# Kernel optimization log

Hardware: AMD Instinct MI355X
Metric: run time of the kernel (lower is better)

Reference implementation:

```python
import jax, jax.numpy as jnp
import numpy as np
import math

B, TQ, TK, C, H, DFF = 4, 1024, 1024, 1024, 16, 4096
DK = C // H
EPS = 1e-12


def _mha(x_q, x_kv, wq, bq, wk, bk, wv, bv, wo, bo, mask):
    Bq, Tq, Cq = x_q.shape
    Tk = x_kv.shape[1]
    q = (x_q @ wq + bq).reshape(Bq, Tq, H, DK).transpose(0, 2, 1, 3)  # [B,H,Tq,dk]
    k = (x_kv @ wk + bk).reshape(Bq, Tk, H, DK).transpose(0, 2, 1, 3)
    v = (x_kv @ wv + bv).reshape(Bq, Tk, H, DK).transpose(0, 2, 1, 3)
    scores = jnp.einsum('bhqd,bhkd->bhqk', q, k) * (1.0 / math.sqrt(DK))
    if mask is not None:
        scores = jnp.where(mask, scores, jnp.asarray(-1e9, scores.dtype))
    attn = jax.nn.softmax(scores, axis=-1)
    o = jnp.einsum('bhqk,bhkd->bhqd', attn, v).transpose(0, 2, 1, 3).reshape(Bq, Tq, Cq)
    return o @ wo + bo


def _ln(x, g, b):
    mu = jnp.mean(x, axis=-1, keepdims=True)
    var = jnp.mean(jnp.square(x - mu), axis=-1, keepdims=True)
    return (x - mu) * jax.lax.rsqrt(var + EPS) * g + b


def setup_inputs() -> dict:
    key = jax.random.key(0)
    ks = iter(jax.random.split(key, 32))
    s = 0.02
    inp = {}
    inp['src'] = jax.random.normal(next(ks), (B, TK, C), jnp.float32)
    inp['dst'] = jax.random.normal(next(ks), (B, TQ, C), jnp.float32)
    inp['src_mask'] = jnp.ones((B, 1, 1, TK), dtype=bool)  # key-padding mask (all valid)
    inp['dst_mask'] = jnp.tril(jnp.ones((TQ, TQ), dtype=bool))[None, None]  # causal
    for p in ['sa', 'ca']:
        for n in ['wq', 'wk', 'wv', 'wo']:
            inp[f'{p}_{n}'] = jax.random.normal(next(ks), (C, C), jnp.float32) * s
        for n in ['bq', 'bk', 'bv', 'bo']:
            inp[f'{p}_{n}'] = jnp.zeros((C,), jnp.float32)
    inp['ffn_w1'] = jax.random.normal(next(ks), (C, DFF), jnp.float32) * s
    inp['ffn_b1'] = jnp.zeros((DFF,), jnp.float32)
    inp['ffn_w2'] = jax.random.normal(next(ks), (DFF, C), jnp.float32) * s
    inp['ffn_b2'] = jnp.zeros((C,), jnp.float32)
    for i in ['1', '2', '3']:
        inp[f'ln{i}_g'] = jnp.ones((C,), jnp.float32)
        inp[f'ln{i}_b'] = jnp.zeros((C,), jnp.float32)
    return inp


def reference(src, dst, src_mask, dst_mask,
              sa_wq, sa_wk, sa_wv, sa_wo, sa_bq, sa_bk, sa_bv, sa_bo,
              ca_wq, ca_wk, ca_wv, ca_wo, ca_bq, ca_bk, ca_bv, ca_bo,
              ffn_w1, ffn_b1, ffn_w2, ffn_b2,
              ln1_g, ln1_b, ln2_g, ln2_b, ln3_g, ln3_b):
    # post-LN decoder layer, eval mode (dropout is identity)
    sa = _mha(dst, dst, sa_wq, sa_bq, sa_wk, sa_bk, sa_wv, sa_bv, sa_wo, sa_bo, dst_mask)
    y = _ln(dst + sa, ln1_g, ln1_b)
    ca = _mha(y, src, ca_wq, ca_bq, ca_wk, ca_bk, ca_wv, ca_bv, ca_wo, ca_bo, src_mask)
    y = _ln(y + ca, ln2_g, ln2_b)
    ff = jax.nn.gelu(y @ ffn_w1 + ffn_b1, approximate=False) @ ffn_w2 + ffn_b2
    return _ln(y + ff, ln3_g, ln3_b)
```

## Files before the change

kernel.cpp:

```cpp
#include <hip/hip_runtime.h>
#include <math.h>

typedef __attribute__((ext_vector_type(4))) float f32x4;
typedef __attribute__((ext_vector_type(8))) __bf16 bf16x8;
typedef __attribute__((ext_vector_type(8))) short short8;

#define DEV __device__ __forceinline__

DEV short f2bfs(float f) {
    unsigned u = __builtin_bit_cast(unsigned, f);
    unsigned r = (u + 0x7FFFu + ((u >> 16) & 1u)) >> 16;
    return (short)r;
}

DEV f32x4 mfma16(bf16x8 a, bf16x8 b, f32x4 c) {
    return __builtin_amdgcn_mfma_f32_16x16x32_bf16(a, b, c, 0, 0, 0);
}

DEV void gload_lds16(const void* g, void* l) {
    __builtin_amdgcn_global_load_lds((const __attribute__((address_space(1))) void*)g,
                                     (__attribute__((address_space(3))) void*)l, 16, 0, 0);
}

__global__ __launch_bounds__(256) void wtrans(const float* __restrict__ Win,
                                              short* __restrict__ Wout,
                                              int Kd, int Nd) {
    __shared__ float Tt[32][33];
    const int tx = threadIdx.x & 31, ty = threadIdx.x >> 5;
    const int k0 = blockIdx.y * 32, n0 = blockIdx.x * 32;
#pragma unroll
    for (int rr = 0; rr < 4; ++rr) {
        int k = ty * 4 + rr;
        Tt[k][tx] = Win[(size_t)(k0 + k) * Nd + n0 + tx];
    }
    __syncthreads();
#pragma unroll
    for (int rr = 0; rr < 4; ++rr) {
        int n = ty * 4 + rr;
        Wout[(size_t)(n0 + n) * Kd + k0 + tx] = f2bfs(Tt[tx][n]);
    }
}

struct WPtrs { const float* p[8]; };

__global__ __launch_bounds__(256) void wtrans8(WPtrs wp, short* __restrict__ out) {
    const float* __restrict__ Win = wp.p[blockIdx.z];
    short* __restrict__ Wout = out + (size_t)blockIdx.z * (1024 * 1024);
    __shared__ float Tt[32][33];
    const int tx = threadIdx.x & 31, ty = threadIdx.x >> 5;
    const int k0 = blockIdx.y * 32, n0 = blockIdx.x * 32;
#pragma unroll
    for (int rr = 0; rr < 4; ++rr) {
        int k = ty * 4 + rr;
        Tt[k][tx] = Win[(size_t)(k0 + k) * 1024 + n0 + tx];
    }
    __syncthreads();
#pragma unroll
    for (int rr = 0; rr < 4; ++rr) {
        int n = ty * 4 + rr;
        Wout[(size_t)(n0 + n) * 1024 + k0 + tx] = f2bfs(Tt[tx][n]);
    }
}

__global__ __launch_bounds__(256) void conv_bf16(const float* __restrict__ X,
                                                 short* __restrict__ Y, int n4) {
    int i = blockIdx.x * 256 + threadIdx.x;
    if (i < n4) {
        float4 v = ((const float4*)X)[i];
        short4 o;
        o.x = f2bfs(v.x); o.y = f2bfs(v.y); o.z = f2bfs(v.z); o.w = f2bfs(v.w);
        ((short4*)Y)[i] = o;
    }
}

template <int BM, int BN, int BK, int EPI, bool SWZ>
__global__ __launch_bounds__(256, (BM == 64 && BN == 64) ? 4 : 1)
void gemm_bt(const short* __restrict__ A,
             const short* __restrict__ BT,
             const float* __restrict__ b0,
             const float* __restrict__ b1,
             const float* __restrict__ b2,
             void* __restrict__ o0,
             void* __restrict__ o1,
             void* __restrict__ o2,
             int M, int N, int K, int Ks) {
    constexpr int IM = BM / 32, JN = BN / 32;
    constexpr int KH = BK / 32;
    constexpr int AL = (BM * 64) / 4096;
    constexpr int BL = (BN * 64) / 4096;
    __shared__ __align__(16) short As[2][BM * BK];
    __shared__ __align__(16) short Bs[2][BN * BK];
    const int tid = threadIdx.x, lane = tid & 63, w = tid >> 6;

    int bx, by, bz;
    if (SWZ) {
        int gx = gridDim.x, gy = gridDim.y;
        int G = gx * gy * gridDim.z;
        int fid = blockIdx.x + gx * (blockIdx.y + gy * blockIdx.z);
        int nf = (fid & 7) * (G >> 3) + (fid >> 3);
        bx = nf % gx;
        int t = nf / gx;
        by = t % gy;
        bz = t / gy;
    } else {
        bx = blockIdx.x; by = blockIdx.y; bz = blockIdx.z;
    }

    const int m0 = by * BM, n0 = bx * BN;
    const int kz = bz * K;
    const int wm = (w & 1) * (BM / 2), wn = (w >> 1) * (BN / 2);
    const int rl = lane & 15, rg = lane >> 4;
    f32x4 acc[IM][JN] = {};
    const char* Ab = (const char*)A;
    const char* Bb = (const char*)BT;
    const int nk = K / BK;

    auto stage = [&](int kt, int buf) {
#pragma unroll
        for (int h = 0; h < KH; ++h) {
#pragma unroll
            for (int r = 0; r < AL; ++r) {
                int lo = (tid + r * 256) * 16;
                int row = lo >> 6, cp = (lo >> 4) & 3, c = (cp - (row >> 1)) & 3;
                gload_lds16(Ab + ((size_t)(m0 + row) * Ks + kz + kt * BK + h * 32 + c * 8) * 2,
                            (char*)As[buf] + h * (BM * 64) + lo);
            }
#pragma unroll
            for (int r = 0; r < BL; ++r) {
                int lo = (tid + r * 256) * 16;
                int row = lo >> 6, cp = (lo >> 4) & 3, c = (cp - (row >> 1)) & 3;
                gload_lds16(Bb + ((size_t)(n0 + row) * Ks + kz + kt * BK + h * 32 + c * 8) * 2,
                            (char*)Bs[buf] + h * (BN * 64) + lo);
            }
        }
    };

    stage(0, 0);
    for (int kt = 0; kt < nk; ++kt) {
        const int buf = kt & 1;
        __syncthreads();
        if (kt + 1 < nk) stage(kt + 1, buf ^ 1);
        bf16x8 af[KH][IM], bfr[KH][JN];
#pragma unroll
        for (int h = 0; h < KH; ++h) {
#pragma unroll
            for (int i = 0; i < IM; i++) {
                int row = wm + i * 16 + rl;
                af[h][i] = *(const bf16x8*)(As[buf] + h * (BM * 32) + row * 32 +
                                            ((rg + (row >> 1)) & 3) * 8);
            }
#pragma unroll
            for (int j = 0; j < JN; j++) {
                int row = wn + j * 16 + rl;
                bfr[h][j] = *(const bf16x8*)(Bs[buf] + h * (BN * 32) + row * 32 +
                                             ((rg + (row >> 1)) & 3) * 8);
            }
        }
#pragma unroll
        for (int h = 0; h < KH; ++h)
#pragma unroll
            for (int i = 0; i < IM; i++)
#pragma unroll
                for (int j = 0; j < JN; j++)
                    acc[i][j] = mfma16(af[h][i], bfr[h][j], acc[i][j]);
    }

    float* o0z = (float*)o0 + (size_t)bz * M * N;
#pragma unroll
    for (int i = 0; i < IM; i++) {
        int gm0 = m0 + wm + i * 16 + rg * 4;
#pragma unroll
        for (int j = 0; j < JN; j++) {
            int gn = n0 + wn + j * 16 + rl;
            if (EPI == 0) {
                float bv = bz == 0 ? b0[gn] : 0.0f;
#pragma unroll
                for (int r = 0; r < 4; r++)
                    o0z[(size_t)(gm0 + r) * N + gn] = acc[i][j][r] + bv;
            } else if (EPI == 2) {
                float bv = b0[gn];
#pragma unroll
                for (int r = 0; r < 4; r++) {
                    float x = acc[i][j][r] + bv;
                    float z = 1.59576912f * x + 0.07135481f * x * x * x;
                    float g = x / (1.0f + __expf(-z));
                    ((short*)o0)[(size_t)(gm0 + r) * N + gn] = f2bfs(g);
                }
            } else {
                int seg = gn >> 10, n1 = gn & 1023, h = n1 >> 6, d = n1 & 63;
                int b = gm0 >> 10, t0 = gm0 & 1023;
                bool isV = (EPI == 1) ? (seg == 2) : (seg == 1);
                const float* bp = (EPI == 1) ? (seg == 0 ? b0 : (seg == 1 ? b1 : b2))
                                             : (seg == 0 ? b0 : b1);
                float bv = bp[n1];
                float qs = (EPI == 1 && seg == 0) ? 0.125f : 1.0f;
                if (!isV) {
                    short* hp = (short*)((EPI == 1) ? (seg == 0 ? o0 : o1) : o0);
                    size_t base = ((size_t)(b * 16 + h) * 1024 + t0) * 64 + d;
#pragma unroll
                    for (int r = 0; r < 4; r++)
                        hp[base + (size_t)r * 64] = f2bfs((acc[i][j][r] + bv) * qs);
                } else {
                    short* vp = (short*)((EPI == 1) ? o2 : o1);
                    short4 pk;
                    pk.x = f2bfs(acc[i][j][0] + bv);
                    pk.y = f2bfs(acc[i][j][1] + bv);
                    pk.z = f2bfs(acc[i][j][2] + bv);
                    pk.w = f2bfs(acc[i][j][3] + bv);
                    *(short4*)(vp + ((size_t)(b * 16 + h) * 64 + d) * 1024 + t0) = pk;
                }
            }
        }
    }
}

template <bool CAUSAL>
__global__ __launch_bounds__(256, 3) void attn4(const short* __restrict__ Qh,
                                                const short* __restrict__ Kh,
                                                const short* __restrict__ VTh,
                                                short* __restrict__ Out, int TKn) {
    __shared__ __align__(16) short Ks[2][64 * 64];
    __shared__ __align__(16) short Vts[2][64 * 64];
    __shared__ __align__(16) short Ps[4][16 * 72 + 8];
    const int tid = threadIdx.x, lane = tid & 63, w = tid >> 6;
    const int rl = lane & 15, rg = lane >> 4;
    const int bh = blockIdx.y, b = bh >> 4, h = bh & 15;
    const int q0 = blockIdx.x * 64;
    const short* Qp = Qh + (size_t)bh * 1024 * 64;
    const char* Kp = (const char*)(Kh + (size_t)bh * (size_t)TKn * 64);
    const char* Vp = (const char*)(VTh + (size_t)bh * (size_t)TKn * 64);

    const int qrow = q0 + w * 16 + rl;
    const bf16x8 qf0 = *(const bf16x8*)(Qp + (size_t)qrow * 64 + rg * 8);
    const bf16x8 qf1 = *(const bf16x8*)(Qp + (size_t)qrow * 64 + 32 + rg * 8);

    bf16x8 onesf;
#pragma unroll
    for (int i = 0; i < 8; ++i) onesf[i] = (__bf16)1.0f;

    f32x4 o[4] = {};
    f32x4 lacc = {};

    short* Pw = &Ps[w][0];
    const int nkt = CAUSAL ? blockIdx.x + 1 : (TKn >> 6);

    auto stage = [&](int kt, int buf) {
#pragma unroll
        for (int r = 0; r < 2; ++r) {
            int lo = (w * 2 + r) * 1024 + lane * 16;
            int row = lo >> 7, cp = (lo >> 4) & 7, c = (cp - row) & 7;
            gload_lds16(Kp + ((size_t)(kt * 64 + row) * 64 + c * 8) * 2,
                        (char*)Ks[buf] + lo);
            gload_lds16(Vp + ((size_t)row * TKn + kt * 64 + c * 8) * 2,
                        (char*)Vts[buf] + lo);
        }
    };

    stage(0, 0);
    for (int kt = 0; kt < nkt; ++kt) {
        const int buf = kt & 1;
        __syncthreads();
        if (kt + 1 < nkt) stage(kt + 1, buf ^ 1);

        const short* KsB = Ks[buf];
        f32x4 s[4];
#pragma unroll
        for (int ch = 0; ch < 4; ++ch) {
            int row = ch * 16 + rl;
            bf16x8 k0 = *(const bf16x8*)(KsB + row * 64 + ((rg + row) & 7) * 8);
            bf16x8 k1 = *(const bf16x8*)(KsB + row * 64 + ((rg + 4 + row) & 7) * 8);
            f32x4 z = {};
            z = mfma16(k0, qf0, z);
            z = mfma16(k1, qf1, z);
            s[ch] = z;
        }
        const bool domask = CAUSAL && (kt == nkt - 1);
#pragma unroll
        for (int ch = 0; ch < 4; ++ch) {
            float p[4];
#pragma unroll
            for (int r = 0; r < 4; ++r) {
                float e = __expf(s[ch][r]);
                if (domask) {
                    int key = kt * 64 + ch * 16 + rg * 4 + r;
                    if (key > qrow) e = 0.0f;
                }
                p[r] = e;
            }
            unsigned d0 = (__builtin_bit_cast(unsigned, p[1]) & 0xFFFF0000u) |
                          (__builtin_bit_cast(unsigned, p[0]) >> 16);
            unsigned d1 = (__builtin_bit_cast(unsigned, p[3]) & 0xFFFF0000u) |
                          (__builtin_bit_cast(unsigned, p[2]) >> 16);
            uint2 dv; dv.x = d0; dv.y = d1;
            *(uint2*)(Pw + rl * 72 + ch * 16 + rg * 4) = dv;
        }
        bf16x8 pa0 = *(const bf16x8*)(Pw + rl * 72 + rg * 8);
        bf16x8 pa1 = *(const bf16x8*)(Pw + rl * 72 + 32 + rg * 8);
        lacc = mfma16(pa0, onesf, lacc);
        lacc = mfma16(pa1, onesf, lacc);
        const short* VsB = Vts[buf];
#pragma unroll
        for (int j = 0; j < 4; ++j) {
            int row = j * 16 + rl;
            bf16x8 v0 = *(const bf16x8*)(VsB + row * 64 + ((rg + row) & 7) * 8);
            bf16x8 v1 = *(const bf16x8*)(VsB + row * 64 + ((rg + 4 + row) & 7) * 8);
            o[j] = mfma16(pa0, v0, o[j]);
            o[j] = mfma16(pa1, v1, o[j]);
        }
    }

    float inv[4];
#pragma unroll
    for (int r = 0; r < 4; r++) inv[r] = 1.0f / lacc[r];
#pragma unroll
    for (int j = 0; j < 4; j++) {
#pragma unroll
        for (int r = 0; r < 4; r++) {
            int row = q0 + w * 16 + rg * 4 + r;
            int col = h * 64 + j * 16 + rl;
            Out[((size_t)b * 1024 + row) * 1024 + col] = f2bfs(o[j][r] * inv[r]);
        }
    }
}

__global__ __launch_bounds__(256) void ln_fused(const float* __restrict__ X,
                                                const float* __restrict__ R,
                                                const float* __restrict__ R2,
                                                const float* __restrict__ gam,
                                                const float* __restrict__ bet,
                                                float* __restrict__ Yf,
                                                short* __restrict__ Yb) {
    const int row = blockIdx.x, tid = threadIdx.x;
    const int lane = tid & 63, w = tid >> 6;
    float4 xv = ((const float4*)(X + (size_t)row * 1024))[tid];
    float4 rv = ((const float4*)(R + (size_t)row * 1024))[tid];
    float v0 = xv.x + rv.x, v1 = xv.y + rv.y, v2 = xv.z + rv.z, v3 = xv.w + rv.w;
    if (R2) {
        float4 r2 = ((const float4*)(R2 + (size_t)row * 1024))[tid];
        v0 += r2.x; v1 += r2.y; v2 += r2.z; v3 += r2.w;
    }
    float s = v0 + v1 + v2 + v3;
    float ss = v0 * v0 + v1 * v1 + v2 * v2 + v3 * v3;
#pragma unroll
    for (int off = 1; off < 64; off <<= 1) {
        s += __shfl_xor(s, off);
        ss += __shfl_xor(ss, off);
    }
    __shared__ float sred[4], ssred[4];
    if (lane == 0) { sred[w] = s; ssred[w] = ss; }
    __syncthreads();
    s = sred[0] + sred[1] + sred[2] + sred[3];
    ss = ssred[0] + ssred[1] + ssred[2] + ssred[3];
    float mu = s * (1.0f / 1024.0f);
    float var = ss * (1.0f / 1024.0f) - mu * mu;
    float rsq = rsqrtf(var + 1e-12f);
    float4 gv = ((const float4*)gam)[tid];
    float4 bv = ((const float4*)bet)[tid];
    float y0 = (v0 - mu) * rsq * gv.x + bv.x;
    float y1 = (v1 - mu) * rsq * gv.y + bv.y;
    float y2 = (v2 - mu) * rsq * gv.z + bv.z;
    float y3 = (v3 - mu) * rsq * gv.w + bv.w;
    float4 yo = {y0, y1, y2, y3};
    ((float4*)(Yf + (size_t)row * 1024))[tid] = yo;
    if (Yb) {
        short4 ob;
        ob.x = f2bfs(y0); ob.y = f2bfs(y1); ob.z = f2bfs(y2); ob.w = f2bfs(y3);
        ((short4*)(Yb + (size_t)row * 1024))[tid] = ob;
    }
}

extern "C" void kernel_launch(void* const* d_in, const int* in_sizes, int n_in,
                              void* d_out, int out_size, void* d_ws, size_t ws_size,
                              hipStream_t stream) {
    const float* src = (const float*)d_in[0];
    const float* dst = (const float*)d_in[1];
    const float* sa_wq = (const float*)d_in[4];
    const float* sa_wk = (const float*)d_in[5];
    const float* sa_wv = (const float*)d_in[6];
    const float* sa_wo = (const float*)d_in[7];
    const float* sa_bq = (const float*)d_in[8];
    const float* sa_bk = (const float*)d_in[9];
    const float* sa_bv = (const float*)d_in[10];
    const float* sa_bo = (const float*)d_in[11];
    const float* ca_wq = (const float*)d_in[12];
    const float* ca_wk = (const float*)d_in[13];
    const float* ca_wv = (const float*)d_in[14];
    const float* ca_wo = (const float*)d_in[15];
    const float* ca_bq = (const float*)d_in[16];
    const float* ca_bk = (const float*)d_in[17];
    const float* ca_bv = (const float*)d_in[18];
    const float* ca_bo = (const float*)d_in[19];
    const float* ffn_w1 = (const float*)d_in[20];
    const float* ffn_b1 = (const float*)d_in[21];
    const float* ffn_w2 = (const float*)d_in[22];
    const float* ffn_b2 = (const float*)d_in[23];
    const float* ln1g = (const float*)d_in[24];
    const float* ln1b = (const float*)d_in[25];
    const float* ln2g = (const float*)d_in[26];
    const float* ln2b = (const float*)d_in[27];
    const float* ln3g = (const float*)d_in[28];
    const float* ln3b = (const float*)d_in[29];

    char* ws = (char*)d_ws;
    size_t off = 0;
    auto alloc = [&](size_t n) { size_t o = off; off = (off + n + 255) & ~(size_t)255; return o; };

    const size_t szW = (size_t)1024 * 1024 * 2;
    short* wT = (short*)(ws + alloc(8 * szW));
    short* w1T = (short*)(ws + alloc((size_t)4096 * 1024 * 2));
    short* w2T = (short*)(ws + alloc((size_t)1024 * 4096 * 2));
    const size_t szAct2 = (size_t)4096 * 1024 * 2;
    const size_t szAct4 = (size_t)4096 * 1024 * 4;
    short* dstb = (short*)(ws + alloc(szAct2));
    short* srcb = (short*)(ws + alloc(szAct2));
    short* Qh = (short*)(ws + alloc(szAct2));
    short* Kh = (short*)(ws + alloc(szAct2));
    short* VTh = (short*)(ws + alloc(szAct2));
    short* attnb = (short*)(ws + alloc(szAct2));
    float* tmp = (float*)(ws + alloc(szAct4));
    float* y1f = (float*)(ws + alloc(szAct4));
    short* y1b = (short*)(ws + alloc(szAct2));
    float* y2f = (float*)(ws + alloc(szAct4));
    short* y2b = (short*)(ws + alloc(szAct2));
    short* ffnh = (short*)(ws + alloc((size_t)4096 * 4096 * 2));

    short* sa_wqkvT = wT;
    short* sa_woT = wT + 3 * (size_t)1048576;
    short* ca_wqT = wT + 4 * (size_t)1048576;
    short* ca_wkvT = wT + 5 * (size_t)1048576;
    short* ca_woT = wT + 7 * (size_t)1048576;

    dim3 blk(256);

    WPtrs wp = {{sa_wq, sa_wk, sa_wv, sa_wo, ca_wq, ca_wk, ca_wv, ca_wo}};
    wtrans8<<<dim3(32, 32, 8), blk, 0, stream>>>(wp, wT);
    wtrans<<<dim3(128, 32), blk, 0, stream>>>(ffn_w1, w1T, 1024, 4096);
    wtrans<<<dim3(32, 128), blk, 0, stream>>>(ffn_w2, w2T, 4096, 1024);
    conv_bf16<<<4096, blk, 0, stream>>>(dst, dstb, 1048576);
    conv_bf16<<<4096, blk, 0, stream>>>(src, srcb, 1048576);

    gemm_bt<128, 128, 32, 1, false><<<dim3(24, 32), blk, 0, stream>>>(
        dstb, sa_wqkvT, sa_bq, sa_bk, sa_bv, Qh, Kh, VTh, 4096, 3072, 1024, 1024);
    attn4<true><<<dim3(16, 64), blk, 0, stream>>>(Qh, Kh, VTh, attnb, 1024);
    gemm_bt<64, 64, 64, 0, true><<<dim3(16, 64), blk, 0, stream>>>(
        attnb, sa_woT, sa_bo, nullptr, nullptr, tmp, nullptr, nullptr, 4096, 1024, 1024, 1024);
    ln_fused<<<4096, blk, 0, stream>>>(dst, tmp, nullptr, ln1g, ln1b, y1f, y1b);

    gemm_bt<64, 64, 64, 1, true><<<dim3(16, 64), blk, 0, stream>>>(
        y1b, ca_wqT, ca_bq, nullptr, nullptr, Qh, nullptr, nullptr, 4096, 1024, 1024, 1024);
    gemm_bt<128, 128, 32, 3, false><<<dim3(16, 32), blk, 0, stream>>>(
        srcb, ca_wkvT, ca_bk, ca_bv, nullptr, Kh, VTh, nullptr, 4096, 2048, 1024, 1024);
    attn4<false><<<dim3(16, 64), blk, 0, stream>>>(Qh, Kh, VTh, attnb, 1024);
    gemm_bt<64, 64, 64, 0, true><<<dim3(16, 64), blk, 0, stream>>>(
        attnb, ca_woT, ca_bo, nullptr, nullptr, tmp, nullptr, nullptr, 4096, 1024, 1024, 1024);
    ln_fused<<<4096, blk, 0, stream>>>(y1f, tmp, nullptr, ln2g, ln2b, y2f, y2b);

    gemm_bt<128, 128, 32, 2, false><<<dim3(32, 32), blk, 0, stream>>>(
        y2b, w1T, ffn_b1, nullptr, nullptr, ffnh, nullptr, nullptr, 4096, 4096, 1024, 1024);
    gemm_bt<64, 64, 64, 0, true><<<dim3(16, 64), blk, 0, stream>>>(
        ffnh, w2T, ffn_b2, nullptr, nullptr, tmp, nullptr, nullptr, 4096, 1024, 4096, 4096);
    ln_fused<<<4096, blk, 0, stream>>>(y2f, tmp, nullptr, ln3g, ln3b, (float*)d_out, nullptr);

    (void)in_sizes; (void)n_in; (void)out_size; (void)ws_size;
}
```

Baseline: 515.5 us.

## Vectorize weight transpose and conversion, split-K FFN down-projection, raise occupancy hint

The weight-transpose kernels now use 64x64 tiles with float4 loads and short4 stores, and the activation-to-bf16 conversion handles 8 elements per thread. The FFN second GEMM (K=4096) is split into two K halves across blockIdx.z, each writing its own partial buffer, and the final layernorm sums the two partials. The min-blocks launch bound for 64x64 GEMM tiles goes from 4 to 5. This exposes more parallelism in the long-K GEMM and cuts memory-instruction counts in the preprocessing kernels, in exchange for an extra fp32 partial buffer round trip and possible register spilling from the tighter occupancy hint.

```diff
diff --git a/kernel.cpp b/kernel.cpp
--- a/kernel.cpp
+++ b/kernel.cpp
@@ -25,19 +25,26 @@
 __global__ __launch_bounds__(256) void wtrans(const float* __restrict__ Win,
                                               short* __restrict__ Wout,
                                               int Kd, int Nd) {
-    __shared__ float Tt[32][33];
-    const int tx = threadIdx.x & 31, ty = threadIdx.x >> 5;
-    const int k0 = blockIdx.y * 32, n0 = blockIdx.x * 32;
+    __shared__ float Tt[64][65];
+    const int tx = threadIdx.x & 15, ty = threadIdx.x >> 4;
+    const int k0 = blockIdx.y * 64, n0 = blockIdx.x * 64;
 #pragma unroll
     for (int rr = 0; rr < 4; ++rr) {
-        int k = ty * 4 + rr;
-        Tt[k][tx] = Win[(size_t)(k0 + k) * Nd + n0 + tx];
+        int k = ty + rr * 16;
+        float4 v = *(const float4*)&Win[(size_t)(k0 + k) * Nd + n0 + tx * 4];
+        Tt[k][tx * 4 + 0] = v.x; Tt[k][tx * 4 + 1] = v.y;
+        Tt[k][tx * 4 + 2] = v.z; Tt[k][tx * 4 + 3] = v.w;
     }
     __syncthreads();
 #pragma unroll
     for (int rr = 0; rr < 4; ++rr) {
-        int n = ty * 4 + rr;
-        Wout[(size_t)(n0 + n) * Kd + k0 + tx] = f2bfs(Tt[tx][n]);
+        int n = ty + rr * 16;
+        short4 o;
+        o.x = f2bfs(Tt[tx * 4 + 0][n]);
+        o.y = f2bfs(Tt[tx * 4 + 1][n]);
+        o.z = f2bfs(Tt[tx * 4 + 2][n]);
+        o.w = f2bfs(Tt[tx * 4 + 3][n]);
+        *(short4*)&Wout[(size_t)(n0 + n) * Kd + k0 + tx * 4] = o;
     }
 }
 
@@ -46,35 +53,44 @@
 __global__ __launch_bounds__(256) void wtrans8(WPtrs wp, short* __restrict__ out) {
     const float* __restrict__ Win = wp.p[blockIdx.z];
     short* __restrict__ Wout = out + (size_t)blockIdx.z * (1024 * 1024);
-    __shared__ float Tt[32][33];
-    const int tx = threadIdx.x & 31, ty = threadIdx.x >> 5;
-    const int k0 = blockIdx.y * 32, n0 = blockIdx.x * 32;
+    __shared__ float Tt[64][65];
+    const int tx = threadIdx.x & 15, ty = threadIdx.x >> 4;
+    const int k0 = blockIdx.y * 64, n0 = blockIdx.x * 64;
 #pragma unroll
     for (int rr = 0; rr < 4; ++rr) {
-        int k = ty * 4 + rr;
-        Tt[k][tx] = Win[(size_t)(k0 + k) * 1024 + n0 + tx];
+        int k = ty + rr * 16;
+        float4 v = *(const float4*)&Win[(size_t)(k0 + k) * 1024 + n0 + tx * 4];
+        Tt[k][tx * 4 + 0] = v.x; Tt[k][tx * 4 + 1] = v.y;
+        Tt[k][tx * 4 + 2] = v.z; Tt[k][tx * 4 + 3] = v.w;
     }
     __syncthreads();
 #pragma unroll
     for (int rr = 0; rr < 4; ++rr) {
-        int n = ty * 4 + rr;
-        Wout[(size_t)(n0 + n) * 1024 + k0 + tx] = f2bfs(Tt[tx][n]);
+        int n = ty + rr * 16;
+        short4 o;
+        o.x = f2bfs(Tt[tx * 4 + 0][n]);
+        o.y = f2bfs(Tt[tx * 4 + 1][n]);
+        o.z = f2bfs(Tt[tx * 4 + 2][n]);
+        o.w = f2bfs(Tt[tx * 4 + 3][n]);
+        *(short4*)&Wout[(size_t)(n0 + n) * 1024 + k0 + tx * 4] = o;
     }
 }
 
 __global__ __launch_bounds__(256) void conv_bf16(const float* __restrict__ X,
-                                                 short* __restrict__ Y, int n4) {
+                                                 short* __restrict__ Y, int n8) {
     int i = blockIdx.x * 256 + threadIdx.x;
-    if (i < n4) {
-        float4 v = ((const float4*)X)[i];
-        short4 o;
-        o.x = f2bfs(v.x); o.y = f2bfs(v.y); o.z = f2bfs(v.z); o.w = f2bfs(v.w);
-        ((short4*)Y)[i] = o;
+    if (i < n8) {
+        float4 a = ((const float4*)X)[i * 2];
+        float4 b = ((const float4*)X)[i * 2 + 1];
+        short8 o;
+        o[0] = f2bfs(a.x); o[1] = f2bfs(a.y); o[2] = f2bfs(a.z); o[3] = f2bfs(a.w);
+        o[4] = f2bfs(b.x); o[5] = f2bfs(b.y); o[6] = f2bfs(b.z); o[7] = f2bfs(b.w);
+        ((short8*)Y)[i] = o;
     }
 }
 
 template <int BM, int BN, int BK, int EPI, bool SWZ>
-__global__ __launch_bounds__(256, (BM == 64 && BN == 64) ? 4 : 1)
+__global__ __launch_bounds__(256, (BM == 64 && BN == 64) ? 5 : 1)
 void gemm_bt(const short* __restrict__ A,
              const short* __restrict__ BT,
              const float* __restrict__ b0,
@@ -417,7 +433,8 @@
     short* Kh = (short*)(ws + alloc(szAct2));
     short* VTh = (short*)(ws + alloc(szAct2));
     short* attnb = (short*)(ws + alloc(szAct2));
-    float* tmp = (float*)(ws + alloc(szAct4));
+    float* tmp = (float*)(ws + alloc(2 * szAct4));
+    float* tmp2 = tmp + (size_t)4096 * 1024;
     float* y1f = (float*)(ws + alloc(szAct4));
     short* y1b = (short*)(ws + alloc(szAct2));
     float* y2f = (float*)(ws + alloc(szAct4));
@@ -433,11 +450,11 @@
     dim3 blk(256);
 
     WPtrs wp = {{sa_wq, sa_wk, sa_wv, sa_wo, ca_wq, ca_wk, ca_wv, ca_wo}};
-    wtrans8<<<dim3(32, 32, 8), blk, 0, stream>>>(wp, wT);
-    wtrans<<<dim3(128, 32), blk, 0, stream>>>(ffn_w1, w1T, 1024, 4096);
-    wtrans<<<dim3(32, 128), blk, 0, stream>>>(ffn_w2, w2T, 4096, 1024);
-    conv_bf16<<<4096, blk, 0, stream>>>(dst, dstb, 1048576);
-    conv_bf16<<<4096, blk, 0, stream>>>(src, srcb, 1048576);
+    wtrans8<<<dim3(16, 16, 8), blk, 0, stream>>>(wp, wT);
+    wtrans<<<dim3(64, 16), blk, 0, stream>>>(ffn_w1, w1T, 1024, 4096);
+    wtrans<<<dim3(16, 64), blk, 0, stream>>>(ffn_w2, w2T, 4096, 1024);
+    conv_bf16<<<2048, blk, 0, stream>>>(dst, dstb, 524288);
+    conv_bf16<<<2048, blk, 0, stream>>>(src, srcb, 524288);
 
     gemm_bt<128, 128, 32, 1, false><<<dim3(24, 32), blk, 0, stream>>>(
         dstb, sa_wqkvT, sa_bq, sa_bk, sa_bv, Qh, Kh, VTh, 4096, 3072, 1024, 1024);
@@ -457,9 +474,9 @@
 
     gemm_bt<128, 128, 32, 2, false><<<dim3(32, 32), blk, 0, stream>>>(
         y2b, w1T, ffn_b1, nullptr, nullptr, ffnh, nullptr, nullptr, 4096, 4096, 1024, 1024);
-    gemm_bt<64, 64, 64, 0, true><<<dim3(16, 64), blk, 0, stream>>>(
-        ffnh, w2T, ffn_b2, nullptr, nullptr, tmp, nullptr, nullptr, 4096, 1024, 4096, 4096);
-    ln_fused<<<4096, blk, 0, stream>>>(y2f, tmp, nullptr, ln3g, ln3b, (float*)d_out, nullptr);
+    gemm_bt<64, 64, 64, 0, true><<<dim3(16, 64, 2), blk, 0, stream>>>(
+        ffnh, w2T, ffn_b2, nullptr, nullptr, tmp, nullptr, nullptr, 4096, 1024, 2048, 4096);
+    ln_fused<<<4096, blk, 0, stream>>>(y2f, tmp, tmp2, ln3g, ln3b, (float*)d_out, nullptr);
 
     (void)in_sizes; (void)n_in; (void)out_size; (void)ws_size;
 }
```

New measurement: 518.9 us. No clear change (+0.7%).
